# Kernel optimization log

Hardware: AMD Instinct MI355X
Metric: run time of the kernel (lower is better)

Reference implementation:

```python
import jax, jax.numpy as jnp
import numpy as np

HIDDEN = 256  # C
STE = 128     # D

def setup_inputs() -> dict:
    key = jax.random.key(0)
    ks = jax.random.split(key, 11)
    B, P, Q, N = 8, 96, 96, 1024
    s = 0.02
    return {
        "enc": jax.random.normal(ks[0], (B, P, N, HIDDEN), jnp.float32),
        "ste_enc": jax.random.normal(ks[1], (B, P, N, STE), jnp.float32),
        "ste_dec": jax.random.normal(ks[2], (B, Q, N, STE), jnp.float32),
        "Wq": jax.random.normal(ks[3], (STE, HIDDEN), jnp.float32) * s,
        "bq": jnp.zeros((HIDDEN,), jnp.float32),
        "Wk": jax.random.normal(ks[4], (STE, HIDDEN), jnp.float32) * s,
        "bk": jnp.zeros((HIDDEN,), jnp.float32),
        "Wv": jax.random.normal(ks[5], (HIDDEN, HIDDEN), jnp.float32) * s,
        "bv": jnp.zeros((HIDDEN,), jnp.float32),
        "Wo": jax.random.normal(ks[6], (HIDDEN, HIDDEN), jnp.float32) * s,
        "bo": jnp.zeros((HIDDEN,), jnp.float32),
    }

def reference(enc, ste_enc, ste_dec, Wq, bq, Wk, bk, Wv, bv, Wo, bo):
    # enc: (B,P,N,C), ste_enc: (B,P,N,D), ste_dec: (B,Q,N,D)
    C = enc.shape[-1]
    q = ste_dec @ Wq + bq          # (B,Q,N,H)
    k = ste_enc @ Wk + bk          # (B,P,N,H)
    v = enc @ Wv + bv              # (B,P,N,H)
    # attention per (batch, node): scores (B,N,Q,P)
    scores = jnp.einsum("bqnh,bpnh->bnqp", q, k) / jnp.sqrt(jnp.float32(C))
    attn = jax.nn.softmax(scores, axis=-1)
    out = jnp.einsum("bnqp,bpnh->bqnh", attn, v)  # (B,Q,N,H)
    out = out @ Wo + bo
    return out  # (B,Q,N,C)
```

## Files before the change

kernel.cpp:

```cpp
#include <hip/hip_runtime.h>
#include <stdint.h>

typedef unsigned short u16;
typedef unsigned int u32;
typedef __attribute__((ext_vector_type(8))) short short8;
typedef __attribute__((ext_vector_type(4))) float f32x4;

#define NTHR 384
#define K2E16 0.09016844005556021f

#define KW_OFF    32768
#define KW_STRIDE 272
#define BIAS_OFF  58880
#define BVO_OFF   59264
#define LDS_TOTAL 60288

static __device__ __forceinline__ u16 f2bf(float f) {
  union { float f; u32 u; } v; v.f = f;
  u32 r = v.u + 0x7FFFu + ((v.u >> 16) & 1u);
  return (u16)(r >> 16);
}

__global__ __launch_bounds__(256) void k_setup(
    const float* __restrict__ Wq, const float* __restrict__ Wk,
    const float* __restrict__ Wv, const float* __restrict__ Wo,
    const float* __restrict__ bq,
    const float* __restrict__ bv, const float* __restrict__ bo,
    u16* __restrict__ WkqF, u16* __restrict__ WvoF, float* __restrict__ bvo) {
  const int ci = blockIdx.x;
  const int co = threadIdx.x;
  float acc = 0.f;
  for (int h = 0; h < 256; ++h) acc += Wv[ci*256 + h] * Wo[h*256 + co];
  const int lanepart = ((ci >> 3) & 3)*16 + (co & 15), e = ci & 7;
  const int idxv = (((ci >> 5)*16 + (co >> 4))*64 + lanepart)*8 + e;
  WvoF[idxv] = f2bf(acc);
  if (ci < 128 && co < 144) {
    float a = 0.f;
    if (co < 128)       { for (int h = 0; h < 256; ++h) a += Wk[ci*256 + h] * Wq[co*256 + h]; }
    else if (co == 128) { for (int h = 0; h < 256; ++h) a += Wk[ci*256 + h] * bq[h]; }
    const int idx = (((ci >> 5)*9 + (co >> 4))*64 + lanepart)*8 + e;
    WkqF[idx] = f2bf(a);
  }
  if (ci == 0) {
    float a2 = 0.f;
    for (int h = 0; h < 256; ++h) a2 += bv[h] * Wo[h*256 + co];
    bvo[co] = a2 + bo[co];
  }
}

__global__ __launch_bounds__(NTHR, 2) void k_attn(
    const float* __restrict__ sdec, const float* __restrict__ senc,
    const float* __restrict__ enc,
    const u16* __restrict__ WkqF, const u16* __restrict__ WvoF,
    const float* __restrict__ bvo, float* __restrict__ out) {
  extern __shared__ char smem[];
  char* wvoL   = smem;
  char* kwL    = smem + KW_OFF;
  char* fragA  = smem + KW_OFF;
  char* fragB  = smem;
  float* biasL = (float*)(smem + BIAS_OFF);
  float* bvoL  = (float*)(smem + BVO_OFF);

  const int n = blockIdx.x, b = blockIdx.y;
  const int tid = threadIdx.x, wave = tid >> 6, lane = tid & 63;
  const int g = lane >> 4, c15 = lane & 15;
  const int prow = 16*wave + c15;

  f32x4 wkq[6];
  #pragma unroll
  for (int i = 0; i < 6; ++i) {
    const int idx = tid + 384*i;
    if (idx < 2048) {
      const int f = idx >> 6, l = idx & 63;
      wkq[i] = ((const f32x4*)WkqF)[((f >> 3)*9 + (f & 7))*64 + l];
    }
  }
  const float* sdp = sdec + ((size_t)((b*96 + prow)*1024 + n))*128 + 8*g;
  const float* sep = senc + ((size_t)((b*96 + prow)*1024 + n))*128 + 8*g;
  float4 sdv[4][2], sev[4][2];
  #pragma unroll
  for (int kt = 0; kt < 4; ++kt) {
    sev[kt][0] = *(const float4*)(sep + 32*kt);
    sev[kt][1] = *(const float4*)(sep + 32*kt + 4);
    sdv[kt][0] = *(const float4*)(sdp + 32*kt);
    sdv[kt][1] = *(const float4*)(sdp + 32*kt + 4);
  }
  const f32x4* wv = (const f32x4*)WvoF;
  f32x4 c0[3];
  #pragma unroll
  for (int i = 0; i < 3; ++i) {
    const int idx = tid + 384*i;
    if (idx < 1024) c0[i] = wv[idx];
  }
  if (tid < 256) bvoL[tid] = bvo[tid];

  {
    f32x4* d = (f32x4*)wvoL;
    #pragma unroll
    for (int i = 0; i < 6; ++i) {
      const int idx = tid + 384*i;
      if (idx < 2048) d[idx] = wkq[i];
    }
  }
  __syncthreads();

  short8 sef[4], sdf[4];
  #pragma unroll
  for (int kt = 0; kt < 4; ++kt) {
    union { u32 u[4]; short8 v; } cv;
    cv.u[0] = (u32)f2bf(sev[kt][0].x) | ((u32)f2bf(sev[kt][0].y) << 16);
    cv.u[1] = (u32)f2bf(sev[kt][0].z) | ((u32)f2bf(sev[kt][0].w) << 16);
    cv.u[2] = (u32)f2bf(sev[kt][1].x) | ((u32)f2bf(sev[kt][1].y) << 16);
    cv.u[3] = (u32)f2bf(sev[kt][1].z) | ((u32)f2bf(sev[kt][1].w) << 16);
    sef[kt] = cv.v;
  }
  #pragma unroll
  for (int kt = 0; kt < 4; ++kt) {
    union { u32 u[4]; short8 v; } cv;
    cv.u[0] = (u32)f2bf(sdv[kt][0].x) | ((u32)f2bf(sdv[kt][0].y) << 16);
    cv.u[1] = (u32)f2bf(sdv[kt][0].z) | ((u32)f2bf(sdv[kt][0].w) << 16);
    cv.u[2] = (u32)f2bf(sdv[kt][1].x) | ((u32)f2bf(sdv[kt][1].y) << 16);
    cv.u[3] = (u32)f2bf(sdv[kt][1].z) | ((u32)f2bf(sdv[kt][1].w) << 16);
    sdf[kt] = cv.v;
  }

  {
    f32x4 acc[9];
    #pragma unroll
    for (int nt = 0; nt < 9; ++nt) acc[nt] = (f32x4)0.f;
    #pragma unroll
    for (int kt = 0; kt < 4; ++kt) {
      #pragma unroll
      for (int nt = 0; nt < 8; ++nt) {
        const short8 bf = *(const short8*)(wvoL + ((kt*8 + nt)*64 + lane)*16);
        acc[nt] = __builtin_amdgcn_mfma_f32_16x16x32_bf16(sef[kt], bf, acc[nt], 0, 0, 0);
      }
      const short8 bf8 = *(const short8*)(WkqF + (size_t)((kt*9 + 8)*64 + lane)*8);
      acc[8] = __builtin_amdgcn_mfma_f32_16x16x32_bf16(sef[kt], bf8, acc[8], 0, 0, 0);
    }
    #pragma unroll
    for (int nt = 0; nt < 8; ++nt) {
      #pragma unroll
      for (int r = 0; r < 4; ++r)
        *(u16*)(kwL + (16*wave + 4*g + r)*KW_STRIDE + 2*(c15 + 16*nt)) = f2bf(acc[nt][r]);
    }
    if (c15 == 0) {
      #pragma unroll
      for (int r = 0; r < 4; ++r) biasL[16*wave + 4*g + r] = acc[8][r];
    }
  }
  __syncthreads();

  {
    f32x4* b0 = (f32x4*)wvoL;
    #pragma unroll
    for (int i = 0; i < 3; ++i) {
      const int idx = tid + 384*i;
      if (idx < 1024) b0[idx] = c0[i];
    }
  }
  f32x4 pf0[3], pf1[3];
  #pragma unroll
  for (int i = 0; i < 3; ++i) {
    const int idx = tid + 384*i;
    if (idx < 1024) pf0[i] = wv[1024 + idx];
  }
  const float* ep = enc + ((size_t)((b*96 + prow)*1024 + n))*256 + 8*g;
  float4 evr[4][2];
  #pragma unroll
  for (int kt = 0; kt < 4; ++kt) {
    evr[kt][0] = *(const float4*)(ep + 32*kt);
    evr[kt][1] = *(const float4*)(ep + 32*kt + 4);
  }

  f32x4 sac[6];
  #pragma unroll
  for (int pt = 0; pt < 6; ++pt) sac[pt] = (f32x4)0.f;
  #pragma unroll
  for (int kt = 0; kt < 4; ++kt) {
    #pragma unroll
    for (int pt = 0; pt < 6; ++pt) {
      const short8 kf = *(const short8*)(kwL + (16*pt + c15)*KW_STRIDE + 16*g + 64*kt);
      sac[pt] = __builtin_amdgcn_mfma_f32_16x16x32_bf16(kf, sdf[kt], sac[pt], 0, 0, 0);
    }
  }
  #pragma unroll
  for (int pt = 0; pt < 6; ++pt)
    #pragma unroll
    for (int r = 0; r < 4; ++r)
      sac[pt][r] += biasL[16*pt + 4*g + r];

  float m = sac[0][0];
  #pragma unroll
  for (int pt = 0; pt < 6; ++pt)
    #pragma unroll
    for (int r = 0; r < 4; ++r) m = fmaxf(m, sac[pt][r]);
  m = fmaxf(m, __shfl_xor(m, 16));
  m = fmaxf(m, __shfl_xor(m, 32));
  float s = 0.f;
  #pragma unroll
  for (int pt = 0; pt < 6; ++pt)
    #pragma unroll
    for (int r = 0; r < 4; ++r) {
      const float e = exp2f((sac[pt][r] - m) * K2E16);
      sac[pt][r] = e; s += e;
    }
  s += __shfl_xor(s, 16);
  s += __shfl_xor(s, 32);
  const float rs = 1.f / s;

  short8 af[3];
  #pragma unroll
  for (int kb = 0; kb < 3; ++kb) {
    union { u32 u[4]; short8 v; } cv;
    cv.u[0] = (u32)f2bf(sac[2*kb][0]*rs)   | ((u32)f2bf(sac[2*kb][1]*rs)   << 16);
    cv.u[1] = (u32)f2bf(sac[2*kb][2]*rs)   | ((u32)f2bf(sac[2*kb][3]*rs)   << 16);
    cv.u[2] = (u32)f2bf(sac[2*kb+1][0]*rs) | ((u32)f2bf(sac[2*kb+1][1]*rs) << 16);
    cv.u[3] = (u32)f2bf(sac[2*kb+1][2]*rs) | ((u32)f2bf(sac[2*kb+1][3]*rs) << 16);
    af[kb] = cv.v;
  }
  __syncthreads();

  f32x4 acc2[16];
  #pragma unroll
  for (int nt = 0; nt < 16; ++nt) acc2[nt] = (f32x4)0.f;
  #pragma unroll
  for (int kt = 0; kt < 8; ++kt) {
    if (kt < 6) {
      const f32x4* src = wv + (kt + 2)*1024;
      if (((kt + 1) & 1) == 0) {
        #pragma unroll
        for (int i = 0; i < 3; ++i) { const int idx = tid + 384*i; if (idx < 1024) pf0[i] = src[idx]; }
      } else {
        #pragma unroll
        for (int i = 0; i < 3; ++i) { const int idx = tid + 384*i; if (idx < 1024) pf1[i] = src[idx]; }
      }
    }
    union { u32 u[4]; short8 v; } cv;
    cv.u[0] = (u32)f2bf(evr[kt & 3][0].x) | ((u32)f2bf(evr[kt & 3][0].y) << 16);
    cv.u[1] = (u32)f2bf(evr[kt & 3][0].z) | ((u32)f2bf(evr[kt & 3][0].w) << 16);
    cv.u[2] = (u32)f2bf(evr[kt & 3][1].x) | ((u32)f2bf(evr[kt & 3][1].y) << 16);
    cv.u[3] = (u32)f2bf(evr[kt & 3][1].z) | ((u32)f2bf(evr[kt & 3][1].w) << 16);
    const short8 a = cv.v;
    if (kt < 4) {
      evr[kt & 3][0] = *(const float4*)(ep + 32*(kt + 4));
      evr[kt & 3][1] = *(const float4*)(ep + 32*(kt + 4) + 4);
    }
    const char* buf = wvoL + (kt & 1)*16384;
    #pragma unroll
    for (int nt = 0; nt < 16; ++nt) {
      const short8 bf = *(const short8*)(buf + ((nt*64 + lane) << 4));
      acc2[nt] = __builtin_amdgcn_mfma_f32_16x16x32_bf16(a, bf, acc2[nt], 0, 0, 0);
    }
    if (kt < 7) {
      f32x4* bw = (f32x4*)(wvoL + ((kt + 1) & 1)*16384);
      if ((kt & 1) == 0) {
        #pragma unroll
        for (int i = 0; i < 3; ++i) { const int idx = tid + 384*i; if (idx < 1024) bw[idx] = pf0[i]; }
      } else {
        #pragma unroll
        for (int i = 0; i < 3; ++i) { const int idx = tid + 384*i; if (idx < 1024) bw[idx] = pf1[i]; }
      }
    }
    __syncthreads();
  }

  const int kb0 = wave >> 1, hi = wave & 1;
  #pragma unroll
  for (int ntl = 0; ntl < 8; ++ntl) {
    uint2 oA, oB;
    const f32x4 vA = acc2[ntl], vB = acc2[8 + ntl];
    oA.x = (u32)f2bf(vA[0]) | ((u32)f2bf(vA[1]) << 16);
    oA.y = (u32)f2bf(vA[2]) | ((u32)f2bf(vA[3]) << 16);
    oB.x = (u32)f2bf(vB[0]) | ((u32)f2bf(vB[1]) << 16);
    oB.y = (u32)f2bf(vB[2]) | ((u32)f2bf(vB[3]) << 16);
    *(uint2*)(fragA + (((ntl*3 + kb0)*64 + lane) << 4) + hi*8) = oA;
    *(uint2*)(fragB + (((ntl*3 + kb0)*64 + lane) << 4) + hi*8) = oB;
  }
  __syncthreads();

  #pragma unroll
  for (int nt = 0; nt < 16; ++nt) {
    const char* fb = (nt < 8) ? fragA : fragB;
    const int ntl = nt & 7;
    f32x4 oa = (f32x4)0.f;
    #pragma unroll
    for (int kb = 0; kb < 3; ++kb) {
      const short8 ef = *(const short8*)(fb + (((ntl*3 + kb)*64 + lane) << 4));
      oa = __builtin_amdgcn_mfma_f32_16x16x32_bf16(af[kb], ef, oa, 0, 0, 0);
    }
    const int c = c15 + 16*nt;
    const float bz = bvoL[c];
    #pragma unroll
    for (int r = 0; r < 4; ++r) {
      const int qi = 16*wave + 4*g + r;
      out[((size_t)((b*96 + qi)*1024 + n))*256 + c] = oa[r] + bz;
    }
  }
}

extern "C" void kernel_launch(void* const* d_in, const int* in_sizes, int n_in,
                              void* d_out, int out_size, void* d_ws, size_t ws_size,
                              hipStream_t stream) {
  const float* enc     = (const float*)d_in[0];
  const float* ste_enc = (const float*)d_in[1];
  const float* ste_dec = (const float*)d_in[2];
  const float* Wq = (const float*)d_in[3];
  const float* bq = (const float*)d_in[4];
  const float* Wk = (const float*)d_in[5];
  const float* Wv = (const float*)d_in[7];
  const float* bv = (const float*)d_in[8];
  const float* Wo = (const float*)d_in[9];
  const float* bo = (const float*)d_in[10];
  float* out = (float*)d_out;

  u16*   WkqF = (u16*)d_ws;
  u16*   WvoF = (u16*)((char*)d_ws + 36864);
  float* bvo  = (float*)((char*)d_ws + 167936);

  k_setup<<<dim3(256), dim3(256), 0, stream>>>(Wq, Wk, Wv, Wo, bq, bv, bo,
                                               WkqF, WvoF, bvo);
  k_attn<<<dim3(1024, 8), dim3(NTHR), LDS_TOTAL, stream>>>(
      ste_dec, ste_enc, enc, WkqF, WvoF, bvo, out);
}
```

Before: 608.9 us.

## Make attention blocks persistent over 16 nodes with resident Wkq in LDS

Each block now handles 16 consecutive nodes in a loop instead of one node per block, shrinking the grid from 8192 to 512 blocks. The Wkq weights (including the bias column) are loaded into LDS once and stay resident, and the next node's ste and enc rows are prefetched during the current node's work. The first Wvo buffers are also reloaded cyclically across iterations. This amortizes weight staging and launch overhead, but LDS use grows to about 146KB, which allows only one block per CU and reduces parallelism. The grid of 512 blocks may also underfill or unbalance the CUs.

```diff
diff --git a/kernel.cpp b/kernel.cpp
--- a/kernel.cpp
+++ b/kernel.cpp
@@ -7,13 +7,16 @@
 typedef __attribute__((ext_vector_type(4))) float f32x4;
 
 #define NTHR 384
+#define JOBS 16
 #define K2E16 0.09016844005556021f
 
-#define KW_OFF    32768
+#define WVO_OFF   36864
+#define KW_OFF    69632
 #define KW_STRIDE 272
-#define BIAS_OFF  58880
-#define BVO_OFF   59264
-#define LDS_TOTAL 60288
+#define FRAG_OFF  95744
+#define BIAS_OFF  144896
+#define BVO_OFF   145280
+#define LDS_TOTAL 146304
 
 static __device__ __forceinline__ u16 f2bf(float f) {
   union { float f; u32 u; } v; v.f = f;
@@ -54,29 +57,29 @@
     const u16* __restrict__ WkqF, const u16* __restrict__ WvoF,
     const float* __restrict__ bvo, float* __restrict__ out) {
   extern __shared__ char smem[];
-  char* wvoL   = smem;
+  char* wkqL   = smem;
+  char* wvoD   = smem + WVO_OFF;
   char* kwL    = smem + KW_OFF;
-  char* fragA  = smem + KW_OFF;
-  char* fragB  = smem;
+  char* fragL  = smem + FRAG_OFF;
   float* biasL = (float*)(smem + BIAS_OFF);
   float* bvoL  = (float*)(smem + BVO_OFF);
 
-  const int n = blockIdx.x, b = blockIdx.y;
+  const int blk = blockIdx.x;
+  const int b = blk >> 6;
+  const int n0 = (blk & 63) << 4;
   const int tid = threadIdx.x, wave = tid >> 6, lane = tid & 63;
   const int g = lane >> 4, c15 = lane & 15;
   const int prow = 16*wave + c15;
+  const size_t rowbase = (size_t)(b*96 + prow)*1024;
+
+  const f32x4* wv = (const f32x4*)WvoF;
 
   f32x4 wkq[6];
   #pragma unroll
-  for (int i = 0; i < 6; ++i) {
-    const int idx = tid + 384*i;
-    if (idx < 2048) {
-      const int f = idx >> 6, l = idx & 63;
-      wkq[i] = ((const f32x4*)WkqF)[((f >> 3)*9 + (f & 7))*64 + l];
-    }
-  }
-  const float* sdp = sdec + ((size_t)((b*96 + prow)*1024 + n))*128 + 8*g;
-  const float* sep = senc + ((size_t)((b*96 + prow)*1024 + n))*128 + 8*g;
+  for (int i = 0; i < 6; ++i) wkq[i] = ((const f32x4*)WkqF)[tid + 384*i];
+
+  const float* sdp = sdec + (rowbase + n0)*128 + 8*g;
+  const float* sep = senc + (rowbase + n0)*128 + 8*g;
   float4 sdv[4][2], sev[4][2];
   #pragma unroll
   for (int kt = 0; kt < 4; ++kt) {
@@ -85,216 +88,234 @@
     sdv[kt][0] = *(const float4*)(sdp + 32*kt);
     sdv[kt][1] = *(const float4*)(sdp + 32*kt + 4);
   }
-  const f32x4* wv = (const f32x4*)WvoF;
-  f32x4 c0[3];
-  #pragma unroll
-  for (int i = 0; i < 3; ++i) {
-    const int idx = tid + 384*i;
-    if (idx < 1024) c0[i] = wv[idx];
-  }
-  if (tid < 256) bvoL[tid] = bvo[tid];
-
-  {
-    f32x4* d = (f32x4*)wvoL;
-    #pragma unroll
-    for (int i = 0; i < 6; ++i) {
-      const int idx = tid + 384*i;
-      if (idx < 2048) d[idx] = wkq[i];
-    }
-  }
-  __syncthreads();
-
-  short8 sef[4], sdf[4];
-  #pragma unroll
-  for (int kt = 0; kt < 4; ++kt) {
-    union { u32 u[4]; short8 v; } cv;
-    cv.u[0] = (u32)f2bf(sev[kt][0].x) | ((u32)f2bf(sev[kt][0].y) << 16);
-    cv.u[1] = (u32)f2bf(sev[kt][0].z) | ((u32)f2bf(sev[kt][0].w) << 16);
-    cv.u[2] = (u32)f2bf(sev[kt][1].x) | ((u32)f2bf(sev[kt][1].y) << 16);
-    cv.u[3] = (u32)f2bf(sev[kt][1].z) | ((u32)f2bf(sev[kt][1].w) << 16);
-    sef[kt] = cv.v;
-  }
-  #pragma unroll
-  for (int kt = 0; kt < 4; ++kt) {
-    union { u32 u[4]; short8 v; } cv;
-    cv.u[0] = (u32)f2bf(sdv[kt][0].x) | ((u32)f2bf(sdv[kt][0].y) << 16);
-    cv.u[1] = (u32)f2bf(sdv[kt][0].z) | ((u32)f2bf(sdv[kt][0].w) << 16);
-    cv.u[2] = (u32)f2bf(sdv[kt][1].x) | ((u32)f2bf(sdv[kt][1].y) << 16);
-    cv.u[3] = (u32)f2bf(sdv[kt][1].z) | ((u32)f2bf(sdv[kt][1].w) << 16);
-    sdf[kt] = cv.v;
-  }
-
-  {
-    f32x4 acc[9];
-    #pragma unroll
-    for (int nt = 0; nt < 9; ++nt) acc[nt] = (f32x4)0.f;
-    #pragma unroll
-    for (int kt = 0; kt < 4; ++kt) {
-      #pragma unroll
-      for (int nt = 0; nt < 8; ++nt) {
-        const short8 bf = *(const short8*)(wvoL + ((kt*8 + nt)*64 + lane)*16);
-        acc[nt] = __builtin_amdgcn_mfma_f32_16x16x32_bf16(sef[kt], bf, acc[nt], 0, 0, 0);
-      }
-      const short8 bf8 = *(const short8*)(WkqF + (size_t)((kt*9 + 8)*64 + lane)*8);
-      acc[8] = __builtin_amdgcn_mfma_f32_16x16x32_bf16(sef[kt], bf8, acc[8], 0, 0, 0);
-    }
-    #pragma unroll
-    for (int nt = 0; nt < 8; ++nt) {
-      #pragma unroll
-      for (int r = 0; r < 4; ++r)
-        *(u16*)(kwL + (16*wave + 4*g + r)*KW_STRIDE + 2*(c15 + 16*nt)) = f2bf(acc[nt][r]);
-    }
-    if (c15 == 0) {
-      #pragma unroll
-      for (int r = 0; r < 4; ++r) biasL[16*wave + 4*g + r] = acc[8][r];
-    }
-  }
-  __syncthreads();
-
-  {
-    f32x4* b0 = (f32x4*)wvoL;
-    #pragma unroll
-    for (int i = 0; i < 3; ++i) {
-      const int idx = tid + 384*i;
-      if (idx < 1024) b0[idx] = c0[i];
-    }
-  }
   f32x4 pf0[3], pf1[3];
   #pragma unroll
   for (int i = 0; i < 3; ++i) {
     const int idx = tid + 384*i;
-    if (idx < 1024) pf0[i] = wv[1024 + idx];
-  }
-  const float* ep = enc + ((size_t)((b*96 + prow)*1024 + n))*256 + 8*g;
+    if (idx < 1024) { pf0[i] = wv[idx]; pf1[i] = wv[1024 + idx]; }
+  }
+  const float* ep = enc + (rowbase + n0)*256 + 8*g;
   float4 evr[4][2];
   #pragma unroll
   for (int kt = 0; kt < 4; ++kt) {
     evr[kt][0] = *(const float4*)(ep + 32*kt);
     evr[kt][1] = *(const float4*)(ep + 32*kt + 4);
   }
-
-  f32x4 sac[6];
-  #pragma unroll
-  for (int pt = 0; pt < 6; ++pt) sac[pt] = (f32x4)0.f;
-  #pragma unroll
-  for (int kt = 0; kt < 4; ++kt) {
-    #pragma unroll
-    for (int pt = 0; pt < 6; ++pt) {
-      const short8 kf = *(const short8*)(kwL + (16*pt + c15)*KW_STRIDE + 16*g + 64*kt);
-      sac[pt] = __builtin_amdgcn_mfma_f32_16x16x32_bf16(kf, sdf[kt], sac[pt], 0, 0, 0);
-    }
-  }
-  #pragma unroll
-  for (int pt = 0; pt < 6; ++pt)
-    #pragma unroll
-    for (int r = 0; r < 4; ++r)
-      sac[pt][r] += biasL[16*pt + 4*g + r];
-
-  float m = sac[0][0];
-  #pragma unroll
-  for (int pt = 0; pt < 6; ++pt)
-    #pragma unroll
-    for (int r = 0; r < 4; ++r) m = fmaxf(m, sac[pt][r]);
-  m = fmaxf(m, __shfl_xor(m, 16));
-  m = fmaxf(m, __shfl_xor(m, 32));
-  float s = 0.f;
-  #pragma unroll
-  for (int pt = 0; pt < 6; ++pt)
-    #pragma unroll
-    for (int r = 0; r < 4; ++r) {
-      const float e = exp2f((sac[pt][r] - m) * K2E16);
-      sac[pt][r] = e; s += e;
-    }
-  s += __shfl_xor(s, 16);
-  s += __shfl_xor(s, 32);
-  const float rs = 1.f / s;
-
-  short8 af[3];
-  #pragma unroll
-  for (int kb = 0; kb < 3; ++kb) {
-    union { u32 u[4]; short8 v; } cv;
-    cv.u[0] = (u32)f2bf(sac[2*kb][0]*rs)   | ((u32)f2bf(sac[2*kb][1]*rs)   << 16);
-    cv.u[1] = (u32)f2bf(sac[2*kb][2]*rs)   | ((u32)f2bf(sac[2*kb][3]*rs)   << 16);
-    cv.u[2] = (u32)f2bf(sac[2*kb+1][0]*rs) | ((u32)f2bf(sac[2*kb+1][1]*rs) << 16);
-    cv.u[3] = (u32)f2bf(sac[2*kb+1][2]*rs) | ((u32)f2bf(sac[2*kb+1][3]*rs) << 16);
-    af[kb] = cv.v;
+  if (tid < 256) bvoL[tid] = bvo[tid];
+
+  {
+    f32x4* d = (f32x4*)wkqL;
+    #pragma unroll
+    for (int i = 0; i < 6; ++i) d[tid + 384*i] = wkq[i];
   }
   __syncthreads();
-
-  f32x4 acc2[16];
-  #pragma unroll
-  for (int nt = 0; nt < 16; ++nt) acc2[nt] = (f32x4)0.f;
-  #pragma unroll
-  for (int kt = 0; kt < 8; ++kt) {
-    if (kt < 6) {
-      const f32x4* src = wv + (kt + 2)*1024;
-      if (((kt + 1) & 1) == 0) {
+  {
+    f32x4* b0 = (f32x4*)wvoD;
+    #pragma unroll
+    for (int i = 0; i < 3; ++i) {
+      const int idx = tid + 384*i;
+      if (idx < 1024) b0[idx] = pf0[i];
+    }
+  }
+
+  #pragma unroll 1
+  for (int j = 0; j < JOBS; ++j) {
+    const int n = n0 + j;
+    const int nn = n0 + ((j + 1) & (JOBS - 1));
+
+    short8 sef[4], sdf[4];
+    #pragma unroll
+    for (int kt = 0; kt < 4; ++kt) {
+      union { u32 u[4]; short8 v; } cv;
+      cv.u[0] = (u32)f2bf(sev[kt][0].x) | ((u32)f2bf(sev[kt][0].y) << 16);
+      cv.u[1] = (u32)f2bf(sev[kt][0].z) | ((u32)f2bf(sev[kt][0].w) << 16);
+      cv.u[2] = (u32)f2bf(sev[kt][1].x) | ((u32)f2bf(sev[kt][1].y) << 16);
+      cv.u[3] = (u32)f2bf(sev[kt][1].z) | ((u32)f2bf(sev[kt][1].w) << 16);
+      sef[kt] = cv.v;
+    }
+    #pragma unroll
+    for (int kt = 0; kt < 4; ++kt) {
+      union { u32 u[4]; short8 v; } cv;
+      cv.u[0] = (u32)f2bf(sdv[kt][0].x) | ((u32)f2bf(sdv[kt][0].y) << 16);
+      cv.u[1] = (u32)f2bf(sdv[kt][0].z) | ((u32)f2bf(sdv[kt][0].w) << 16);
+      cv.u[2] = (u32)f2bf(sdv[kt][1].x) | ((u32)f2bf(sdv[kt][1].y) << 16);
+      cv.u[3] = (u32)f2bf(sdv[kt][1].z) | ((u32)f2bf(sdv[kt][1].w) << 16);
+      sdf[kt] = cv.v;
+    }
+    {
+      const float* sdpn = sdec + (rowbase + nn)*128 + 8*g;
+      const float* sepn = senc + (rowbase + nn)*128 + 8*g;
+      #pragma unroll
+      for (int kt = 0; kt < 4; ++kt) {
+        sev[kt][0] = *(const float4*)(sepn + 32*kt);
+        sev[kt][1] = *(const float4*)(sepn + 32*kt + 4);
+        sdv[kt][0] = *(const float4*)(sdpn + 32*kt);
+        sdv[kt][1] = *(const float4*)(sdpn + 32*kt + 4);
+      }
+    }
+
+    {
+      f32x4 acc[9];
+      #pragma unroll
+      for (int nt = 0; nt < 9; ++nt) acc[nt] = (f32x4)0.f;
+      #pragma unroll
+      for (int kt = 0; kt < 4; ++kt) {
         #pragma unroll
-        for (int i = 0; i < 3; ++i) { const int idx = tid + 384*i; if (idx < 1024) pf0[i] = src[idx]; }
-      } else {
+        for (int nt = 0; nt < 9; ++nt) {
+          const short8 bf = *(const short8*)(wkqL + ((kt*9 + nt)*64 + lane)*16);
+          acc[nt] = __builtin_amdgcn_mfma_f32_16x16x32_bf16(sef[kt], bf, acc[nt], 0, 0, 0);
+        }
+      }
+      #pragma unroll
+      for (int nt = 0; nt < 8; ++nt) {
         #pragma unroll
-        for (int i = 0; i < 3; ++i) { const int idx = tid + 384*i; if (idx < 1024) pf1[i] = src[idx]; }
-      }
-    }
-    union { u32 u[4]; short8 v; } cv;
-    cv.u[0] = (u32)f2bf(evr[kt & 3][0].x) | ((u32)f2bf(evr[kt & 3][0].y) << 16);
-    cv.u[1] = (u32)f2bf(evr[kt & 3][0].z) | ((u32)f2bf(evr[kt & 3][0].w) << 16);
-    cv.u[2] = (u32)f2bf(evr[kt & 3][1].x) | ((u32)f2bf(evr[kt & 3][1].y) << 16);
-    cv.u[3] = (u32)f2bf(evr[kt & 3][1].z) | ((u32)f2bf(evr[kt & 3][1].w) << 16);
-    const short8 a = cv.v;
-    if (kt < 4) {
-      evr[kt & 3][0] = *(const float4*)(ep + 32*(kt + 4));
-      evr[kt & 3][1] = *(const float4*)(ep + 32*(kt + 4) + 4);
-    }
-    const char* buf = wvoL + (kt & 1)*16384;
+        for (int r = 0; r < 4; ++r)
+          *(u16*)(kwL + (16*wave + 4*g + r)*KW_STRIDE + 2*(c15 + 16*nt)) = f2bf(acc[nt][r]);
+      }
+      if (c15 == 0) {
+        #pragma unroll
+        for (int r = 0; r < 4; ++r) biasL[16*wave + 4*g + r] = acc[8][r];
+      }
+    }
+    __syncthreads();
+
+    f32x4 sac[6];
+    #pragma unroll
+    for (int pt = 0; pt < 6; ++pt) sac[pt] = (f32x4)0.f;
+    #pragma unroll
+    for (int kt = 0; kt < 4; ++kt) {
+      #pragma unroll
+      for (int pt = 0; pt < 6; ++pt) {
+        const short8 kf = *(const short8*)(kwL + (16*pt + c15)*KW_STRIDE + 16*g + 64*kt);
+        sac[pt] = __builtin_amdgcn_mfma_f32_16x16x32_bf16(kf, sdf[kt], sac[pt], 0, 0, 0);
+      }
+    }
+    #pragma unroll
+    for (int pt = 0; pt < 6; ++pt)
+      #pragma unroll
+      for (int r = 0; r < 4; ++r)
+        sac[pt][r] += biasL[16*pt + 4*g + r];
+
+    float m = sac[0][0];
+    #pragma unroll
+    for (int pt = 0; pt < 6; ++pt)
+      #pragma unroll
+      for (int r = 0; r < 4; ++r) m = fmaxf(m, sac[pt][r]);
+    m = fmaxf(m, __shfl_xor(m, 16));
+    m = fmaxf(m, __shfl_xor(m, 32));
+    float s = 0.f;
+    #pragma unroll
+    for (int pt = 0; pt < 6; ++pt)
+      #pragma unroll
+      for (int r = 0; r < 4; ++r) {
+        const float e = exp2f((sac[pt][r] - m) * K2E16);
+        sac[pt][r] = e; s += e;
+      }
+    s += __shfl_xor(s, 16);
+    s += __shfl_xor(s, 32);
+    const float rs = 1.f / s;
+
+    short8 af[3];
+    #pragma unroll
+    for (int kb = 0; kb < 3; ++kb) {
+      union { u32 u[4]; short8 v; } cv;
+      cv.u[0] = (u32)f2bf(sac[2*kb][0]*rs)   | ((u32)f2bf(sac[2*kb][1]*rs)   << 16);
+      cv.u[1] = (u32)f2bf(sac[2*kb][2]*rs)   | ((u32)f2bf(sac[2*kb][3]*rs)   << 16);
+      cv.u[2] = (u32)f2bf(sac[2*kb+1][0]*rs) | ((u32)f2bf(sac[2*kb+1][1]*rs) << 16);
+      cv.u[3] = (u32)f2bf(sac[2*kb+1][2]*rs) | ((u32)f2bf(sac[2*kb+1][3]*rs) << 16);
+      af[kb] = cv.v;
+    }
+    __syncthreads();
+
+    f32x4 acc2[16];
+    #pragma unroll
+    for (int nt = 0; nt < 16; ++nt) acc2[nt] = (f32x4)0.f;
+    #pragma unroll
+    for (int kt = 0; kt < 8; ++kt) {
+      {
+        const f32x4* src = wv + ((kt + 2) & 7)*1024;
+        if ((kt & 1) == 0) {
+          #pragma unroll
+          for (int i = 0; i < 3; ++i) { const int idx = tid + 384*i; if (idx < 1024) pf0[i] = src[idx]; }
+        } else {
+          #pragma unroll
+          for (int i = 0; i < 3; ++i) { const int idx = tid + 384*i; if (idx < 1024) pf1[i] = src[idx]; }
+        }
+      }
+      union { u32 u[4]; short8 v; } cv;
+      cv.u[0] = (u32)f2bf(evr[kt & 3][0].x) | ((u32)f2bf(evr[kt & 3][0].y) << 16);
+      cv.u[1] = (u32)f2bf(evr[kt & 3][0].z) | ((u32)f2bf(evr[kt & 3][0].w) << 16);
+      cv.u[2] = (u32)f2bf(evr[kt & 3][1].x) | ((u32)f2bf(evr[kt & 3][1].y) << 16);
+      cv.u[3] = (u32)f2bf(evr[kt & 3][1].z) | ((u32)f2bf(evr[kt & 3][1].w) << 16);
+      const short8 a = cv.v;
+      if (kt < 4) {
+        evr[kt & 3][0] = *(const float4*)(ep + 32*(kt + 4));
+        evr[kt & 3][1] = *(const float4*)(ep + 32*(kt + 4) + 4);
+      }
+      const char* buf = wvoD + (kt & 1)*16384;
+      #pragma unroll
+      for (int nt = 0; nt < 16; ++nt) {
+        const short8 bf = *(const short8*)(buf + ((nt*64 + lane) << 4));
+        acc2[nt] = __builtin_amdgcn_mfma_f32_16x16x32_bf16(a, bf, acc2[nt], 0, 0, 0);
+      }
+      if (kt < 7) {
+        f32x4* bw = (f32x4*)(wvoD + ((kt + 1) & 1)*16384);
+        if (((kt + 1) & 1) == 0) {
+          #pragma unroll
+          for (int i = 0; i < 3; ++i) { const int idx = tid + 384*i; if (idx < 1024) bw[idx] = pf0[i]; }
+        } else {
+          #pragma unroll
+          for (int i = 0; i < 3; ++i) { const int idx = tid + 384*i; if (idx < 1024) bw[idx] = pf1[i]; }
+        }
+      }
+      __syncthreads();
+    }
+
+    {
+      f32x4* b0 = (f32x4*)wvoD;
+      #pragma unroll
+      for (int i = 0; i < 3; ++i) { const int idx = tid + 384*i; if (idx < 1024) b0[idx] = pf0[i]; }
+    }
+    const int kb0 = wave >> 1, hi = wave & 1;
     #pragma unroll
     for (int nt = 0; nt < 16; ++nt) {
-      const short8 bf = *(const short8*)(buf + ((nt*64 + lane) << 4));
-      acc2[nt] = __builtin_amdgcn_mfma_f32_16x16x32_bf16(a, bf, acc2[nt], 0, 0, 0);
-    }
-    if (kt < 7) {
-      f32x4* bw = (f32x4*)(wvoL + ((kt + 1) & 1)*16384);
-      if ((kt & 1) == 0) {
-        #pragma unroll
-        for (int i = 0; i < 3; ++i) { const int idx = tid + 384*i; if (idx < 1024) bw[idx] = pf0[i]; }
-      } else {
-        #pragma unroll
-        for (int i = 0; i < 3; ++i) { const int idx = tid + 384*i; if (idx < 1024) bw[idx] = pf1[i]; }
-      }
+      uint2 o;
+      const f32x4 v = acc2[nt];
+      o.x = (u32)f2bf(v[0]) | ((u32)f2bf(v[1]) << 16);
+      o.y = (u32)f2bf(v[2]) | ((u32)f2bf(v[3]) << 16);
+      *(uint2*)(fragL + (((nt*3 + kb0)*64 + lane) << 4) + hi*8) = o;
+    }
+    {
+      const float* epn = enc + (rowbase + nn)*256 + 8*g;
+      #pragma unroll
+      for (int kt = 0; kt < 4; ++kt) {
+        evr[kt][0] = *(const float4*)(epn + 32*kt);
+        evr[kt][1] = *(const float4*)(epn + 32*kt + 4);
+      }
+      ep = epn;
+    }
+    {
+      f32x4* b1 = (f32x4*)(wvoD + 16384);
+      #pragma unroll
+      for (int i = 0; i < 3; ++i) { const int idx = tid + 384*i; if (idx < 1024) b1[idx] = pf1[i]; }
     }
     __syncthreads();
-  }
-
-  const int kb0 = wave >> 1, hi = wave & 1;
-  #pragma unroll
-  for (int ntl = 0; ntl < 8; ++ntl) {
-    uint2 oA, oB;
-    const f32x4 vA = acc2[ntl], vB = acc2[8 + ntl];
-    oA.x = (u32)f2bf(vA[0]) | ((u32)f2bf(vA[1]) << 16);
-    oA.y = (u32)f2bf(vA[2]) | ((u32)f2bf(vA[3]) << 16);
-    oB.x = (u32)f2bf(vB[0]) | ((u32)f2bf(vB[1]) << 16);
-    oB.y = (u32)f2bf(vB[2]) | ((u32)f2bf(vB[3]) << 16);
-    *(uint2*)(fragA + (((ntl*3 + kb0)*64 + lane) << 4) + hi*8) = oA;
-    *(uint2*)(fragB + (((ntl*3 + kb0)*64 + lane) << 4) + hi*8) = oB;
-  }
-  __syncthreads();
-
-  #pragma unroll
-  for (int nt = 0; nt < 16; ++nt) {
-    const char* fb = (nt < 8) ? fragA : fragB;
-    const int ntl = nt & 7;
-    f32x4 oa = (f32x4)0.f;
-    #pragma unroll
-    for (int kb = 0; kb < 3; ++kb) {
-      const short8 ef = *(const short8*)(fb + (((ntl*3 + kb)*64 + lane) << 4));
-      oa = __builtin_amdgcn_mfma_f32_16x16x32_bf16(af[kb], ef, oa, 0, 0, 0);
-    }
-    const int c = c15 + 16*nt;
-    const float bz = bvoL[c];
-    #pragma unroll
-    for (int r = 0; r < 4; ++r) {
-      const int qi = 16*wave + 4*g + r;
-      out[((size_t)((b*96 + qi)*1024 + n))*256 + c] = oa[r] + bz;
+
+    #pragma unroll
+    for (int nt = 0; nt < 16; ++nt) {
+      f32x4 oa = (f32x4)0.f;
+      #pragma unroll
+      for (int kb = 0; kb < 3; ++kb) {
+        const short8 ef = *(const short8*)(fragL + (((nt*3 + kb)*64 + lane) << 4));
+        oa = __builtin_amdgcn_mfma_f32_16x16x32_bf16(af[kb], ef, oa, 0, 0, 0);
+      }
+      const int c = c15 + 16*nt;
+      const float bz = bvoL[c];
+      #pragma unroll
+      for (int r = 0; r < 4; ++r) {
+        const int qi = 16*wave + 4*g + r;
+        out[((size_t)((b*96 + qi)*1024 + n))*256 + c] = oa[r] + bz;
+      }
     }
   }
 }
@@ -318,8 +339,11 @@
   u16*   WvoF = (u16*)((char*)d_ws + 36864);
   float* bvo  = (float*)((char*)d_ws + 167936);
 
+  (void)hipFuncSetAttribute((const void*)k_attn,
+        hipFuncAttributeMaxDynamicSharedMemorySize, LDS_TOTAL);
+
   k_setup<<<dim3(256), dim3(256), 0, stream>>>(Wq, Wk, Wv, Wo, bq, bv, bo,
                                                WkqF, WvoF, bvo);
-  k_attn<<<dim3(1024, 8), dim3(NTHR), LDS_TOTAL, stream>>>(
+  k_attn<<<dim3(512), dim3(NTHR), LDS_TOTAL, stream>>>(
       ste_dec, ste_enc, enc, WkqF, WvoF, bvo, out);
 }
```

Result: slower. 975.7 us (+60.3%).
